# Performance work log

Hardware: AMD Instinct MI355X
Metric: run time of the kernel (lower is better)

## Reference

```python
import jax, jax.numpy as jnp
import numpy as np

H = 4  # num_heads

def setup_inputs() -> dict:
    key = jax.random.key(0)
    ks = jax.random.split(key, 9)
    B, S, D = 8, 2048, 256
    x = jax.random.normal(ks[0], (B, S, D), dtype=jnp.float32)
    scale = 1.0 / np.sqrt(D)
    Wq = jax.random.normal(ks[1], (D, D), dtype=jnp.float32) * scale
    bq = jnp.zeros((D,), dtype=jnp.float32)
    Wk = jax.random.normal(ks[2], (D, D), dtype=jnp.float32) * scale
    bk = jnp.zeros((D,), dtype=jnp.float32)
    Wv = jax.random.normal(ks[3], (D, D), dtype=jnp.float32) * scale
    bv = jnp.zeros((D,), dtype=jnp.float32)
    Wo = jax.random.normal(ks[4], (D, D), dtype=jnp.float32) * scale
    bo = jnp.zeros((D,), dtype=jnp.float32)
    return {"x": x, "Wq": Wq, "bq": bq, "Wk": Wk, "bk": bk,
            "Wv": Wv, "bv": bv, "Wo": Wo, "bo": bo}

def reference(x, Wq, bq, Wk, bk, Wv, bv, Wo, bo):
    B, S, D = x.shape
    hd = D // H
    inv_scale = 1.0 / jnp.sqrt(jnp.asarray(hd, x.dtype))
    # projections: torch Linear is x @ W.T + b; weights here stored as (D, D) used as x @ W + b
    def split_heads(t):
        return t.reshape(B, S, H, hd).transpose(0, 2, 1, 3)  # [B,H,S,hd]
    Q = split_heads(x @ Wq + bq)
    K = split_heads(x @ Wk + bk)
    V = split_heads(x @ Wv + bv)
    scores = jnp.einsum('bhqd,bhkd->bhqk', Q, K) * inv_scale  # [B,H,S,S]
    attn = jax.nn.softmax(scores, axis=-1)
    # dropout is identity in eval mode
    ctx = jnp.einsum('bhqk,bhkd->bhqd', attn, V)
    ctx = ctx.transpose(0, 2, 1, 3).reshape(B, S, D)
    return ctx @ Wo + bo
```

## Files before the change

### kernel.cpp

```cpp
#include <hip/hip_runtime.h>


typedef unsigned short u16;
typedef __bf16 bf16x8 __attribute__((ext_vector_type(8)));
typedef float  f32x4  __attribute__((ext_vector_type(4)));
typedef unsigned int u32x4 __attribute__((ext_vector_type(4)));
typedef unsigned int u32x2 __attribute__((ext_vector_type(2)));

#define LOG2E   1.4426950408889634f
#define ATTN_SC (0.125f * LOG2E)
#define PSTR    2097152
#define WPSTR   32768
#define WZSTR   65536

__device__ __forceinline__ u16 f2b(float f) {
  unsigned u = __builtin_bit_cast(unsigned, f);
  u += 0x7FFFu + ((u >> 16) & 1u);
  return (u16)(u >> 16);
}
__device__ __forceinline__ float b2f(u16 b) {
  return __builtin_bit_cast(float, (unsigned)b << 16);
}
__device__ __forceinline__ float b2f_hi(unsigned u) {
  return __builtin_bit_cast(float, u & 0xFFFF0000u);
}
__device__ __forceinline__ float b2f_lo(unsigned u) {
  return __builtin_bit_cast(float, u << 16);
}
__device__ __forceinline__ unsigned pack_trunc(float a, float b) {
  return (__builtin_bit_cast(unsigned, a) >> 16) | (__builtin_bit_cast(unsigned, b) & 0xFFFF0000u);
}
__device__ __forceinline__ unsigned pack_rne(float a, float b) {
  return (unsigned)f2b(a) | ((unsigned)f2b(b) << 16);
}
__device__ __forceinline__ f32x4 mfma16(bf16x8 a, bf16x8 b, f32x4 c) {
  return __builtin_amdgcn_mfma_f32_16x16x32_bf16(a, b, c, 0, 0, 0);
}
__device__ __forceinline__ void cp16(const u16* g, u16* l) {
  __builtin_amdgcn_global_load_lds((const __attribute__((address_space(1))) void*)g,
                                   (__attribute__((address_space(3))) void*)l, 16, 0, 0);
}

template <typename T>
__global__ __launch_bounds__(256) void prep(const T* __restrict__ x,
                                            const T* __restrict__ W0, const T* __restrict__ W1,
                                            const T* __restrict__ W2, const T* __restrict__ W3,
                                            const T* __restrict__ b0, const T* __restrict__ b1,
                                            const T* __restrict__ b2, const T* __restrict__ b3,
                                            u16* __restrict__ xp, u16* __restrict__ WTp,
                                            float* __restrict__ biasf) {
  int bid = blockIdx.x;
  if (bid < 4096) {
    int i0 = (bid * 256 + threadIdx.x) * 4;
    int row = i0 >> 8, col = i0 & 255;
    int p = col >> 7, pc = col & 127;
    u16* o = xp + (size_t)p * PSTR + (size_t)row * 128 + pc;
#pragma unroll
    for (int j = 0; j < 4; ++j) {
      if constexpr (sizeof(T) == 4) o[j] = f2b((float)x[i0 + j]);
      else                          o[j] = (u16)x[i0 + j];
    }
  } else {
    bid -= 4096;
    const int z = bid >> 8;
    const T* W = z == 0 ? W0 : z == 1 ? W1 : z == 2 ? W2 : W3;
    const T* b = z == 0 ? b0 : z == 1 ? b1 : z == 2 ? b2 : b3;
    int idx = (bid & 255) * 256 + threadIdx.x;
    int k = idx >> 8, n = idx & 255;
    u16 wb;
    if constexpr (sizeof(T) == 4) wb = f2b((float)W[k * 256 + n]);
    else                          wb = (u16)W[k * 256 + n];
    WTp[z * WZSTR + (k >> 7) * WPSTR + n * 128 + (k & 127)] = wb;
    if (idx < 256) {
      float bv;
      if constexpr (sizeof(T) == 4) bv = (float)b[idx];
      else                          bv = b2f((u16)b[idx]);
      biasf[z * 256 + idx] = bv;
    }
  }
}

__global__ __launch_bounds__(256, 2) void qkv_gemm(const u16* __restrict__ xp, const u16* __restrict__ WTp,
                                                   const float* __restrict__ biasf,
                                                   u16* __restrict__ Qw, u16* __restrict__ Kw,
                                                   u16* __restrict__ VTg) {
  __shared__ __align__(16) u16 Al[256 * 128];
  __shared__ __align__(16) u16 Bl[64 * 128];
  const int tid = threadIdx.x, w = tid >> 6, lane = tid & 63;
  const int l16 = lane & 15, quad = lane >> 4;
  const int z = blockIdx.z, n0 = blockIdx.y * 64, m0 = blockIdx.x * 256;
  const u16* Ab = xp + (size_t)m0 * 128;
  const u16* Bb = WTp + z * WZSTR + (size_t)n0 * 128;
  f32x4 acc[4][4];
#pragma unroll
  for (int mm = 0; mm < 4; ++mm)
#pragma unroll
    for (int nb = 0; nb < 4; ++nb) acc[mm][nb] = (f32x4){0.f, 0.f, 0.f, 0.f};

#pragma unroll
  for (int p = 0; p < 2; ++p) {
    __syncthreads();
    const u16* Ap = Ab + (size_t)p * PSTR;
    const u16* Bp = Bb + p * WPSTR;
#pragma unroll
    for (int i = 0; i < 16; ++i) {
      int slot = i * 256 + w * 64 + lane;
      int row = slot >> 4, pc = slot & 15, c = pc ^ (row & 15);
      cp16(Ap + (size_t)row * 128 + c * 8, Al + (i * 256 + w * 64) * 8);
    }
#pragma unroll
    for (int i = 0; i < 4; ++i) {
      int slot = i * 256 + w * 64 + lane;
      int row = slot >> 4, pc = slot & 15, c = pc ^ (row & 15);
      cp16(Bp + (size_t)row * 128 + c * 8, Bl + (i * 256 + w * 64) * 8);
    }
    __syncthreads();
#pragma unroll
    for (int kc = 0; kc < 4; ++kc) {
      int ch = ((kc * 4 + quad) ^ l16) * 8;
      bf16x8 a[4], b[4];
#pragma unroll
      for (int mm = 0; mm < 4; ++mm)
        a[mm] = *(const bf16x8*)&Al[(w * 64 + mm * 16 + l16) * 128 + ch];
#pragma unroll
      for (int nb = 0; nb < 4; ++nb)
        b[nb] = *(const bf16x8*)&Bl[(nb * 16 + l16) * 128 + ch];
#pragma unroll
      for (int mm = 0; mm < 4; ++mm)
#pragma unroll
        for (int nb = 0; nb < 4; ++nb)
          acc[mm][nb] = mfma16(a[mm], b[nb], acc[mm][nb]);
    }
  }

  const float* bp = biasf + z * 256;
  const int bb = m0 >> 11, s0 = m0 & 2047, h = blockIdx.y;
  if (z < 2) {
    u16* dst = (z == 0) ? Qw : Kw;
    const float sc = (z == 0) ? ATTN_SC : 1.0f;
#pragma unroll
    for (int mm = 0; mm < 4; ++mm)
#pragma unroll
      for (int nb = 0; nb < 4; ++nb) {
        int d = nb * 16 + l16;
        float bv = bp[n0 + d];
#pragma unroll
        for (int r = 0; r < 4; ++r) {
          int s = s0 + w * 64 + mm * 16 + quad * 4 + r;
          dst[(((size_t)(bb * 4 + h) * 2048) + s) * 64 + d] = f2b((acc[mm][nb][r] + bv) * sc);
        }
      }
  } else {
    __syncthreads();
#pragma unroll
    for (int mm = 0; mm < 4; ++mm)
#pragma unroll
      for (int nb = 0; nb < 4; ++nb) {
        int d = nb * 16 + l16;
        float bv = bp[n0 + d];
        f32x4 v = acc[mm][nb];
        u32x2 dd = { pack_rne(v[0] + bv, v[1] + bv), pack_rne(v[2] + bv, v[3] + bv) };
        int cch = w * 8 + mm * 2 + (quad >> 1);
        *(u32x2*)&Al[d * 256 + ((cch ^ (d & 31))) * 8 + (quad & 1) * 4] = dd;
      }
    __syncthreads();
#pragma unroll
    for (int i = 0; i < 8; ++i) {
      int slot = i * 256 + tid;
      int d = slot >> 5, pc = slot & 31;
      u32x4 vv = *(const u32x4*)&Al[d * 256 + ((pc ^ (d & 31))) * 8];
      *(u32x4*)(VTg + (((size_t)(bb * 4 + h) * 64) + d) * 2048 + s0 + pc * 8) = vv;
    }
  }
}

template <bool OUT_BF16>
__global__ __launch_bounds__(256) void out_gemm(const u16* __restrict__ ctxp, const u16* __restrict__ WTp,
                                                const float* __restrict__ bo, void* __restrict__ outv) {
  __shared__ __align__(16) u16 Al[128 * 128];
  __shared__ __align__(16) u16 Bl[64 * 128];
  const int tid = threadIdx.x, w = tid >> 6, lane = tid & 63;
  const int l16 = lane & 15, quad = lane >> 4;
  const int n0 = blockIdx.y * 64, m0 = blockIdx.x * 128;
  const u16* Ab = ctxp + (size_t)m0 * 128;
  const u16* Bb = WTp + 3 * WZSTR + (size_t)n0 * 128;
  f32x4 acc[2][4];
#pragma unroll
  for (int mm = 0; mm < 2; ++mm)
#pragma unroll
    for (int nb = 0; nb < 4; ++nb) acc[mm][nb] = (f32x4){0.f, 0.f, 0.f, 0.f};

#pragma unroll
  for (int p = 0; p < 2; ++p) {
    __syncthreads();
    const u16* Ap = Ab + (size_t)p * PSTR;
    const u16* Bp = Bb + p * WPSTR;
#pragma unroll
    for (int i = 0; i < 8; ++i) {
      int slot = i * 256 + w * 64 + lane;
      int row = slot >> 4, pc = slot & 15, c = pc ^ (row & 15);
      cp16(Ap + (size_t)row * 128 + c * 8, Al + (i * 256 + w * 64) * 8);
    }
#pragma unroll
    for (int i = 0; i < 4; ++i) {
      int slot = i * 256 + w * 64 + lane;
      int row = slot >> 4, pc = slot & 15, c = pc ^ (row & 15);
      cp16(Bp + (size_t)row * 128 + c * 8, Bl + (i * 256 + w * 64) * 8);
    }
    __syncthreads();
#pragma unroll
    for (int kc = 0; kc < 4; ++kc) {
      int ch = ((kc * 4 + quad) ^ l16) * 8;
      bf16x8 a0 = *(const bf16x8*)&Al[(w * 32 + l16) * 128 + ch];
      bf16x8 a1 = *(const bf16x8*)&Al[(w * 32 + 16 + l16) * 128 + ch];
#pragma unroll
      for (int nb = 0; nb < 4; ++nb) {
        bf16x8 b = *(const bf16x8*)&Bl[(nb * 16 + l16) * 128 + ch];
        acc[0][nb] = mfma16(a0, b, acc[0][nb]);
        acc[1][nb] = mfma16(a1, b, acc[1][nb]);
      }
    }
  }
#pragma unroll
  for (int mm = 0; mm < 2; ++mm)
#pragma unroll
    for (int nb = 0; nb < 4; ++nb) {
      int n = n0 + nb * 16 + l16;
      float bv = bo[n];
#pragma unroll
      for (int r = 0; r < 4; ++r) {
        size_t m = m0 + w * 32 + mm * 16 + quad * 4 + r;
        float v = acc[mm][nb][r] + bv;
        if constexpr (OUT_BF16) ((u16*)outv)[m * 256 + n] = f2b(v);
        else                    ((float*)outv)[m * 256 + n] = v;
      }
    }
}

__global__ __launch_bounds__(256, 3) void attn(const u16* __restrict__ Q, const u16* __restrict__ K,
                                               const u16* __restrict__ VT,
                                               u16* __restrict__ P0, u16* __restrict__ P1,
                                               float* __restrict__ dnb) {
  __shared__ __align__(16) u16 Kt[2][64 * 64];
  __shared__ __align__(16) u16 VTt[2][64 * 64];
  __shared__ __align__(16) u16 Pt[4][2][16 * 64];
  const int tid = threadIdx.x;
  const int w = tid >> 6, lane = tid & 63;
  const int l16 = lane & 15, quad = lane >> 4;
  const int bh = blockIdx.y, q0 = blockIdx.x * 128, z = blockIdx.z;
  const u16* Qp = Q + (size_t)bh * 2048 * 64;
  const u16* Kp = K + (size_t)bh * 2048 * 64 + (size_t)z * 1024 * 64;
  const u16* Vp = VT + (size_t)bh * 64 * 2048 + z * 1024;

  bf16x8 qf[2][2];
#pragma unroll
  for (int g = 0; g < 2; ++g) {
    int qrow = q0 + w * 32 + g * 16 + l16;
    qf[g][0] = *(const bf16x8*)(Qp + (size_t)qrow * 64 + quad * 8);
    qf[g][1] = *(const bf16x8*)(Qp + (size_t)qrow * 64 + 32 + quad * 8);
  }

  f32x4 acc[2][4];
#pragma unroll
  for (int g = 0; g < 2; ++g)
#pragma unroll
    for (int nb = 0; nb < 4; ++nb) acc[g][nb] = (f32x4){0.f, 0.f, 0.f, 0.f};
  float dn[2] = {0.f, 0.f};

  const int sl0 = tid, sl1 = 256 + tid;
  const int r0 = sl0 >> 3, c0 = (sl0 & 7) ^ (r0 & 7);
  const int r1 = sl1 >> 3, c1 = (sl1 & 7) ^ (r1 & 7);

#define STAGE(kt_, buf_)                                                                   \
  do {                                                                                     \
    cp16(Kp + (size_t)((kt_) * 64 + r0) * 64 + c0 * 8, &Kt[buf_][(w * 64) * 8]);           \
    cp16(Kp + (size_t)((kt_) * 64 + r1) * 64 + c1 * 8, &Kt[buf_][(256 + w * 64) * 8]);     \
    cp16(Vp + (size_t)r0 * 2048 + (kt_) * 64 + c0 * 8, &VTt[buf_][(w * 64) * 8]);          \
    cp16(Vp + (size_t)r1 * 2048 + (kt_) * 64 + c1 * 8, &VTt[buf_][(256 + w * 64) * 8]);    \
  } while (0)

  STAGE(0, 0);

  for (int kt = 0; kt < 16; ++kt) {
    const int buf = kt & 1;
    __builtin_amdgcn_s_waitcnt(0x0F70 );
    __asm__ __volatile__("" ::: "memory");
    __builtin_amdgcn_s_barrier();
    __asm__ __volatile__("" ::: "memory");
    if (kt < 15) STAGE(kt + 1, buf ^ 1);

    const u16* KtB = Kt[buf];
    const u16* VtB = VTt[buf];

    bf16x8 vbr[2][4];
#pragma unroll
    for (int m = 0; m < 2; ++m)
#pragma unroll
      for (int nbD = 0; nbD < 4; ++nbD)
        vbr[m][nbD] = *(const bf16x8*)&VtB[(nbD * 16 + l16) * 64 + (((m * 4 + quad) ^ (l16 & 7))) * 8];

    f32x4 st[2][4];
#pragma unroll
    for (int g = 0; g < 2; ++g)
#pragma unroll
      for (int nb = 0; nb < 4; ++nb) st[g][nb] = (f32x4){0.f, 0.f, 0.f, 0.f};
#pragma unroll
    for (int kc = 0; kc < 2; ++kc) {
#pragma unroll
      for (int nbK = 0; nbK < 4; ++nbK) {
        bf16x8 a = *(const bf16x8*)&KtB[(nbK * 16 + l16) * 64 + (((kc * 4 + quad) ^ (l16 & 7))) * 8];
        st[0][nbK] = mfma16(a, qf[0][kc], st[0][nbK]);
        st[1][nbK] = mfma16(a, qf[1][kc], st[1][nbK]);
      }
    }

#pragma unroll
    for (int g = 0; g < 2; ++g) {
      u16* Ptg = Pt[w][g];
#pragma unroll
      for (int nbK = 0; nbK < 4; ++nbK) {
        float p0 = exp2f(st[g][nbK][0]), p1 = exp2f(st[g][nbK][1]);
        float p2 = exp2f(st[g][nbK][2]), p3 = exp2f(st[g][nbK][3]);
        dn[g] += (p0 + p1) + (p2 + p3);
        u32x2 dd = { pack_trunc(p0, p1), pack_trunc(p2, p3) };
        int cch = nbK * 2 + (quad >> 1);
        *(u32x2*)&Ptg[l16 * 64 + ((cch ^ (l16 & 7))) * 8 + (quad & 1) * 4] = dd;
      }
    }

#pragma unroll
    for (int m = 0; m < 2; ++m) {
#pragma unroll
      for (int g = 0; g < 2; ++g) {
        bf16x8 pb = *(const bf16x8*)&Pt[w][g][l16 * 64 + (((m * 4 + quad) ^ (l16 & 7))) * 8];
#pragma unroll
        for (int nbD = 0; nbD < 4; ++nbD)
          acc[g][nbD] = mfma16(vbr[m][nbD], pb, acc[g][nbD]);
      }
    }
  }
#undef STAGE

  u16* pdst = z ? P1 : P0;
#pragma unroll
  for (int g = 0; g < 2; ++g) {
    float d = dn[g];
    d += __shfl_xor(d, 16);
    d += __shfl_xor(d, 32);
    dn[g] = d;
    if (quad == 0)
      dnb[z * 65536 + bh * 2048 + q0 + w * 32 + g * 16 + l16] = d;
  }

#pragma unroll
  for (int g = 0; g < 2; ++g) {
    u16* Ptg = Pt[w][g];
#pragma unroll
    for (int nbD = 0; nbD < 4; ++nbD) {
      f32x4 v = acc[g][nbD];
      u32x2 dd = { pack_rne(v[0], v[1]), pack_rne(v[2], v[3]) };
      int cch = nbD * 2 + (quad >> 1);
      *(u32x2*)&Ptg[l16 * 64 + ((cch ^ (l16 & 7))) * 8 + (quad & 1) * 4] = dd;
    }
  }
#pragma unroll
  for (int cc = 0; cc < 4; ++cc) {
    int slot = cc * 64 + lane;
    int row = slot >> 3, pc = slot & 7;
    u32x4 vv = *(const u32x4*)&Pt[w][0][row * 64 + ((pc ^ (row & 7))) * 8];
    size_t qg = q0 + w * 32 + row;
    *(u32x4*)(pdst + (((size_t)bh * 2048) + qg) * 64 + pc * 8) = vv;
  }
}

__global__ __launch_bounds__(256) void combine(const u16* __restrict__ p0, const u16* __restrict__ p1,
                                               const float* __restrict__ dnb, u16* __restrict__ ctxp) {
  int t = blockIdx.x * 256 + threadIdx.x;
  int chunk = t & 7, q = (t >> 3) & 2047, bh = t >> 14;
  size_t idx = ((((size_t)bh * 2048) + q) * 64) + chunk * 8;
  u32x4 a = *(const u32x4*)(p0 + idx);
  u32x4 b = *(const u32x4*)(p1 + idx);
  float l = 1.0f / (dnb[bh * 2048 + q] + dnb[65536 + bh * 2048 + q]);
  u32x4 o;
#pragma unroll
  for (int i = 0; i < 4; ++i) {
    float lo = (b2f_lo(a[i]) + b2f_lo(b[i])) * l;
    float hi = (b2f_hi(a[i]) + b2f_hi(b[i])) * l;
    o[i] = pack_rne(lo, hi);
  }
  int bb = bh >> 2, h = bh & 3, p = h >> 1, pcol = (h & 1) * 64;
  size_t m = (size_t)bb * 2048 + q;
  *(u32x4*)(ctxp + (size_t)p * PSTR + m * 128 + pcol + chunk * 8) = o;
}

extern "C" void kernel_launch(void* const* d_in, const int* in_sizes, int n_in,
                              void* d_out, int out_size, void* d_ws, size_t ws_size,
                              hipStream_t stream) {
  bool f32in = true;
  {
    void* basep = nullptr; size_t sz = 0;
    hipError_t e = hipMemGetAddressRange((hipDeviceptr_t*)&basep, &sz, (hipDeviceptr_t)d_in[0]);
    if (e == hipSuccess && sz > 0) f32in = sz >= (size_t)in_sizes[0] * 4;
    else f32in = false;
  }

  char* ws = (char*)d_ws;
  u16*   xp    = (u16*)(ws + 0);
  u16*   WTp   = (u16*)(ws + 8388608);
  float* biasf = (float*)(ws + 8912896);
  u16*   Qw    = (u16*)(ws + 8916992);
  u16*   Kw    = (u16*)(ws + 17305600);
  u16*   VTg   = (u16*)(ws + 25694208);
  float* dnb   = (float*)(ws + 34082816);
  u16*   part0 = xp;
  u16*   part1 = (u16*)d_out;
  u16*   ctxp  = Qw;

  if (f32in) {
    prep<float><<<5120, 256, 0, stream>>>(
        (const float*)d_in[0],
        (const float*)d_in[1], (const float*)d_in[3], (const float*)d_in[5], (const float*)d_in[7],
        (const float*)d_in[2], (const float*)d_in[4], (const float*)d_in[6], (const float*)d_in[8],
        xp, WTp, biasf);
  } else {
    prep<u16><<<5120, 256, 0, stream>>>(
        (const u16*)d_in[0],
        (const u16*)d_in[1], (const u16*)d_in[3], (const u16*)d_in[5], (const u16*)d_in[7],
        (const u16*)d_in[2], (const u16*)d_in[4], (const u16*)d_in[6], (const u16*)d_in[8],
        xp, WTp, biasf);
  }
  qkv_gemm<<<dim3(64, 4, 3), 256, 0, stream>>>(xp, WTp, biasf, Qw, Kw, VTg);
  attn<<<dim3(16, 32, 2), 256, 0, stream>>>(Qw, Kw, VTg, part0, part1, dnb);
  combine<<<2048, 256, 0, stream>>>(part0, part1, dnb, ctxp);
  if (f32in) out_gemm<false><<<dim3(128, 4), 256, 0, stream>>>(ctxp, WTp, biasf + 3 * 256, d_out);
  else       out_gemm<true ><<<dim3(128, 4), 256, 0, stream>>>(ctxp, WTp, biasf + 3 * 256, d_out);
}
```

Measured before the change: 173.6 us.

## Fuse x conversion into QKV GEMM and split-combine into output GEMM

```diff
diff --git a/kernel.cpp b/kernel.cpp
--- a/kernel.cpp
+++ b/kernel.cpp
@@ -9,7 +9,6 @@
 
 #define LOG2E   1.4426950408889634f
 #define ATTN_SC (0.125f * LOG2E)
-#define PSTR    2097152
 #define WPSTR   32768
 #define WZSTR   65536
 
@@ -42,45 +41,30 @@
 }
 
 template <typename T>
-__global__ __launch_bounds__(256) void prep(const T* __restrict__ x,
-                                            const T* __restrict__ W0, const T* __restrict__ W1,
+__global__ __launch_bounds__(256) void prep(const T* __restrict__ W0, const T* __restrict__ W1,
                                             const T* __restrict__ W2, const T* __restrict__ W3,
                                             const T* __restrict__ b0, const T* __restrict__ b1,
                                             const T* __restrict__ b2, const T* __restrict__ b3,
-                                            u16* __restrict__ xp, u16* __restrict__ WTp,
-                                            float* __restrict__ biasf) {
-  int bid = blockIdx.x;
-  if (bid < 4096) {
-    int i0 = (bid * 256 + threadIdx.x) * 4;
-    int row = i0 >> 8, col = i0 & 255;
-    int p = col >> 7, pc = col & 127;
-    u16* o = xp + (size_t)p * PSTR + (size_t)row * 128 + pc;
-#pragma unroll
-    for (int j = 0; j < 4; ++j) {
-      if constexpr (sizeof(T) == 4) o[j] = f2b((float)x[i0 + j]);
-      else                          o[j] = (u16)x[i0 + j];
-    }
-  } else {
-    bid -= 4096;
-    const int z = bid >> 8;
-    const T* W = z == 0 ? W0 : z == 1 ? W1 : z == 2 ? W2 : W3;
-    const T* b = z == 0 ? b0 : z == 1 ? b1 : z == 2 ? b2 : b3;
-    int idx = (bid & 255) * 256 + threadIdx.x;
-    int k = idx >> 8, n = idx & 255;
-    u16 wb;
-    if constexpr (sizeof(T) == 4) wb = f2b((float)W[k * 256 + n]);
-    else                          wb = (u16)W[k * 256 + n];
-    WTp[z * WZSTR + (k >> 7) * WPSTR + n * 128 + (k & 127)] = wb;
-    if (idx < 256) {
-      float bv;
-      if constexpr (sizeof(T) == 4) bv = (float)b[idx];
-      else                          bv = b2f((u16)b[idx]);
-      biasf[z * 256 + idx] = bv;
-    }
-  }
-}
-
-__global__ __launch_bounds__(256, 2) void qkv_gemm(const u16* __restrict__ xp, const u16* __restrict__ WTp,
+                                            u16* __restrict__ WTp, float* __restrict__ biasf) {
+  const int z = blockIdx.x >> 8;
+  const T* W = z == 0 ? W0 : z == 1 ? W1 : z == 2 ? W2 : W3;
+  const T* b = z == 0 ? b0 : z == 1 ? b1 : z == 2 ? b2 : b3;
+  int idx = (blockIdx.x & 255) * 256 + threadIdx.x;
+  int k = idx >> 8, n = idx & 255;
+  u16 wb;
+  if constexpr (sizeof(T) == 4) wb = f2b((float)W[k * 256 + n]);
+  else                          wb = (u16)W[k * 256 + n];
+  WTp[z * WZSTR + (k >> 7) * WPSTR + n * 128 + (k & 127)] = wb;
+  if (idx < 256) {
+    float bv;
+    if constexpr (sizeof(T) == 4) bv = (float)b[idx];
+    else                          bv = b2f((u16)b[idx]);
+    biasf[z * 256 + idx] = bv;
+  }
+}
+
+template <typename T>
+__global__ __launch_bounds__(256, 2) void qkv_gemm(const T* __restrict__ x, const u16* __restrict__ WTp,
                                                    const float* __restrict__ biasf,
                                                    u16* __restrict__ Qw, u16* __restrict__ Kw,
                                                    u16* __restrict__ VTg) {
@@ -89,7 +73,6 @@
   const int tid = threadIdx.x, w = tid >> 6, lane = tid & 63;
   const int l16 = lane & 15, quad = lane >> 4;
   const int z = blockIdx.z, n0 = blockIdx.y * 64, m0 = blockIdx.x * 256;
-  const u16* Ab = xp + (size_t)m0 * 128;
   const u16* Bb = WTp + z * WZSTR + (size_t)n0 * 128;
   f32x4 acc[4][4];
 #pragma unroll
@@ -100,19 +83,28 @@
 #pragma unroll
   for (int p = 0; p < 2; ++p) {
     __syncthreads();
-    const u16* Ap = Ab + (size_t)p * PSTR;
     const u16* Bp = Bb + p * WPSTR;
 #pragma unroll
     for (int i = 0; i < 16; ++i) {
-      int slot = i * 256 + w * 64 + lane;
+      int slot = i * 256 + tid;
       int row = slot >> 4, pc = slot & 15, c = pc ^ (row & 15);
-      cp16(Ap + (size_t)row * 128 + c * 8, Al + (i * 256 + w * 64) * 8);
+      const T* src = x + (size_t)(m0 + row) * 256 + p * 128 + c * 8;
+      u32x4 dd;
+      if constexpr (sizeof(T) == 4) {
+        f32x4 v0 = *(const f32x4*)src;
+        f32x4 v1 = *(const f32x4*)(src + 4);
+        dd = (u32x4){ pack_rne(v0[0], v0[1]), pack_rne(v0[2], v0[3]),
+                      pack_rne(v1[0], v1[1]), pack_rne(v1[2], v1[3]) };
+      } else {
+        dd = *(const u32x4*)src;
+      }
+      *(u32x4*)&Al[slot * 8] = dd;
     }
 #pragma unroll
     for (int i = 0; i < 4; ++i) {
-      int slot = i * 256 + w * 64 + lane;
+      int slot = i * 256 + tid;
       int row = slot >> 4, pc = slot & 15, c = pc ^ (row & 15);
-      cp16(Bp + (size_t)row * 128 + c * 8, Bl + (i * 256 + w * 64) * 8);
+      cp16(Bp + (size_t)row * 128 + c * 8, Bl + slot * 8);
     }
     __syncthreads();
 #pragma unroll
@@ -174,76 +166,13 @@
   }
 }
 
-template <bool OUT_BF16>
-__global__ __launch_bounds__(256) void out_gemm(const u16* __restrict__ ctxp, const u16* __restrict__ WTp,
-                                                const float* __restrict__ bo, void* __restrict__ outv) {
-  __shared__ __align__(16) u16 Al[128 * 128];
-  __shared__ __align__(16) u16 Bl[64 * 128];
-  const int tid = threadIdx.x, w = tid >> 6, lane = tid & 63;
-  const int l16 = lane & 15, quad = lane >> 4;
-  const int n0 = blockIdx.y * 64, m0 = blockIdx.x * 128;
-  const u16* Ab = ctxp + (size_t)m0 * 128;
-  const u16* Bb = WTp + 3 * WZSTR + (size_t)n0 * 128;
-  f32x4 acc[2][4];
-#pragma unroll
-  for (int mm = 0; mm < 2; ++mm)
-#pragma unroll
-    for (int nb = 0; nb < 4; ++nb) acc[mm][nb] = (f32x4){0.f, 0.f, 0.f, 0.f};
-
-#pragma unroll
-  for (int p = 0; p < 2; ++p) {
-    __syncthreads();
-    const u16* Ap = Ab + (size_t)p * PSTR;
-    const u16* Bp = Bb + p * WPSTR;
-#pragma unroll
-    for (int i = 0; i < 8; ++i) {
-      int slot = i * 256 + w * 64 + lane;
-      int row = slot >> 4, pc = slot & 15, c = pc ^ (row & 15);
-      cp16(Ap + (size_t)row * 128 + c * 8, Al + (i * 256 + w * 64) * 8);
-    }
-#pragma unroll
-    for (int i = 0; i < 4; ++i) {
-      int slot = i * 256 + w * 64 + lane;
-      int row = slot >> 4, pc = slot & 15, c = pc ^ (row & 15);
-      cp16(Bp + (size_t)row * 128 + c * 8, Bl + (i * 256 + w * 64) * 8);
-    }
-    __syncthreads();
-#pragma unroll
-    for (int kc = 0; kc < 4; ++kc) {
-      int ch = ((kc * 4 + quad) ^ l16) * 8;
-      bf16x8 a0 = *(const bf16x8*)&Al[(w * 32 + l16) * 128 + ch];
-      bf16x8 a1 = *(const bf16x8*)&Al[(w * 32 + 16 + l16) * 128 + ch];
-#pragma unroll
-      for (int nb = 0; nb < 4; ++nb) {
-        bf16x8 b = *(const bf16x8*)&Bl[(nb * 16 + l16) * 128 + ch];
-        acc[0][nb] = mfma16(a0, b, acc[0][nb]);
-        acc[1][nb] = mfma16(a1, b, acc[1][nb]);
-      }
-    }
-  }
-#pragma unroll
-  for (int mm = 0; mm < 2; ++mm)
-#pragma unroll
-    for (int nb = 0; nb < 4; ++nb) {
-      int n = n0 + nb * 16 + l16;
-      float bv = bo[n];
-#pragma unroll
-      for (int r = 0; r < 4; ++r) {
-        size_t m = m0 + w * 32 + mm * 16 + quad * 4 + r;
-        float v = acc[mm][nb][r] + bv;
-        if constexpr (OUT_BF16) ((u16*)outv)[m * 256 + n] = f2b(v);
-        else                    ((float*)outv)[m * 256 + n] = v;
-      }
-    }
-}
-
-__global__ __launch_bounds__(256, 3) void attn(const u16* __restrict__ Q, const u16* __restrict__ K,
+__global__ __launch_bounds__(256, 4) void attn(const u16* __restrict__ Q, const u16* __restrict__ K,
                                                const u16* __restrict__ VT,
                                                u16* __restrict__ P0, u16* __restrict__ P1,
                                                float* __restrict__ dnb) {
   __shared__ __align__(16) u16 Kt[2][64 * 64];
   __shared__ __align__(16) u16 VTt[2][64 * 64];
-  __shared__ __align__(16) u16 Pt[4][2][16 * 64];
+  __shared__ __align__(16) u16 Pt[4][16 * 64];
   const int tid = threadIdx.x;
   const int w = tid >> 6, lane = tid & 63;
   const int l16 = lane & 15, quad = lane >> 4;
@@ -251,6 +180,7 @@
   const u16* Qp = Q + (size_t)bh * 2048 * 64;
   const u16* Kp = K + (size_t)bh * 2048 * 64 + (size_t)z * 1024 * 64;
   const u16* Vp = VT + (size_t)bh * 64 * 2048 + z * 1024;
+  u16* Ptw = Pt[w];
 
   bf16x8 qf[2][2];
 #pragma unroll
@@ -292,13 +222,6 @@
     const u16* KtB = Kt[buf];
     const u16* VtB = VTt[buf];
 
-    bf16x8 vbr[2][4];
-#pragma unroll
-    for (int m = 0; m < 2; ++m)
-#pragma unroll
-      for (int nbD = 0; nbD < 4; ++nbD)
-        vbr[m][nbD] = *(const bf16x8*)&VtB[(nbD * 16 + l16) * 64 + (((m * 4 + quad) ^ (l16 & 7))) * 8];
-
     f32x4 st[2][4];
 #pragma unroll
     for (int g = 0; g < 2; ++g)
@@ -314,9 +237,15 @@
       }
     }
 
+    bf16x8 vbr[2][4];
+#pragma unroll
+    for (int m = 0; m < 2; ++m)
+#pragma unroll
+      for (int nbD = 0; nbD < 4; ++nbD)
+        vbr[m][nbD] = *(const bf16x8*)&VtB[(nbD * 16 + l16) * 64 + (((m * 4 + quad) ^ (l16 & 7))) * 8];
+
 #pragma unroll
     for (int g = 0; g < 2; ++g) {
-      u16* Ptg = Pt[w][g];
 #pragma unroll
       for (int nbK = 0; nbK < 4; ++nbK) {
         float p0 = exp2f(st[g][nbK][0]), p1 = exp2f(st[g][nbK][1]);
@@ -324,15 +253,11 @@
         dn[g] += (p0 + p1) + (p2 + p3);
         u32x2 dd = { pack_trunc(p0, p1), pack_trunc(p2, p3) };
         int cch = nbK * 2 + (quad >> 1);
-        *(u32x2*)&Ptg[l16 * 64 + ((cch ^ (l16 & 7))) * 8 + (quad & 1) * 4] = dd;
-      }
-    }
-
-#pragma unroll
-    for (int m = 0; m < 2; ++m) {
-#pragma unroll
-      for (int g = 0; g < 2; ++g) {
-        bf16x8 pb = *(const bf16x8*)&Pt[w][g][l16 * 64 + (((m * 4 + quad) ^ (l16 & 7))) * 8];
+        *(u32x2*)&Ptw[l16 * 64 + ((cch ^ (l16 & 7))) * 8 + (quad & 1) * 4] = dd;
+      }
+#pragma unroll
+      for (int m = 0; m < 2; ++m) {
+        bf16x8 pb = *(const bf16x8*)&Ptw[l16 * 64 + (((m * 4 + quad) ^ (l16 & 7))) * 8];
 #pragma unroll
         for (int nbD = 0; nbD < 4; ++nbD)
           acc[g][nbD] = mfma16(vbr[m][nbD], pb, acc[g][nbD]);
@@ -347,34 +272,32 @@
     float d = dn[g];
     d += __shfl_xor(d, 16);
     d += __shfl_xor(d, 32);
-    dn[g] = d;
     if (quad == 0)
       dnb[z * 65536 + bh * 2048 + q0 + w * 32 + g * 16 + l16] = d;
   }
 
 #pragma unroll
   for (int g = 0; g < 2; ++g) {
-    u16* Ptg = Pt[w][g];
 #pragma unroll
     for (int nbD = 0; nbD < 4; ++nbD) {
       f32x4 v = acc[g][nbD];
       u32x2 dd = { pack_rne(v[0], v[1]), pack_rne(v[2], v[3]) };
       int cch = nbD * 2 + (quad >> 1);
-      *(u32x2*)&Ptg[l16 * 64 + ((cch ^ (l16 & 7))) * 8 + (quad & 1) * 4] = dd;
-    }
-  }
-#pragma unroll
-  for (int cc = 0; cc < 4; ++cc) {
-    int slot = cc * 64 + lane;
-    int row = slot >> 3, pc = slot & 7;
-    u32x4 vv = *(const u32x4*)&Pt[w][0][row * 64 + ((pc ^ (row & 7))) * 8];
-    size_t qg = q0 + w * 32 + row;
-    *(u32x4*)(pdst + (((size_t)bh * 2048) + qg) * 64 + pc * 8) = vv;
+      *(u32x2*)&Ptw[l16 * 64 + ((cch ^ (l16 & 7))) * 8 + (quad & 1) * 4] = dd;
+    }
+#pragma unroll
+    for (int cc = 0; cc < 2; ++cc) {
+      int slot = cc * 64 + lane;
+      int row = slot >> 3, pc = slot & 7;
+      u32x4 vv = *(const u32x4*)&Ptw[row * 64 + ((pc ^ (row & 7))) * 8];
+      size_t qg = q0 + w * 32 + g * 16 + row;
+      *(u32x4*)(pdst + (((size_t)bh * 2048) + qg) * 64 + pc * 8) = vv;
+    }
   }
 }
 
 __global__ __launch_bounds__(256) void combine(const u16* __restrict__ p0, const u16* __restrict__ p1,
-                                               const float* __restrict__ dnb, u16* __restrict__ ctxp) {
+                                               const float* __restrict__ dnb, u16* __restrict__ ctxc) {
   int t = blockIdx.x * 256 + threadIdx.x;
   int chunk = t & 7, q = (t >> 3) & 2047, bh = t >> 14;
   size_t idx = ((((size_t)bh * 2048) + q) * 64) + chunk * 8;
@@ -388,9 +311,85 @@
     float hi = (b2f_hi(a[i]) + b2f_hi(b[i])) * l;
     o[i] = pack_rne(lo, hi);
   }
-  int bb = bh >> 2, h = bh & 3, p = h >> 1, pcol = (h & 1) * 64;
-  size_t m = (size_t)bb * 2048 + q;
-  *(u32x4*)(ctxp + (size_t)p * PSTR + m * 128 + pcol + chunk * 8) = o;
+  *(u32x4*)(ctxc + idx) = o;
+}
+
+template <bool OUT_BF16, bool MERGED>
+__global__ __launch_bounds__(256) void out_gemm(const u16* __restrict__ p0, const u16* __restrict__ p1,
+                                                const float* __restrict__ dnb,
+                                                const u16* __restrict__ WTp,
+                                                const float* __restrict__ bo, void* __restrict__ outv) {
+  __shared__ __align__(16) u16 Al[128 * 128];
+  __shared__ __align__(16) u16 Bl[64 * 128];
+  const int tid = threadIdx.x, w = tid >> 6, lane = tid & 63;
+  const int l16 = lane & 15, quad = lane >> 4;
+  const int n0 = blockIdx.y * 64, m0 = blockIdx.x * 128;
+  const u16* Bb = WTp + 3 * WZSTR + (size_t)n0 * 128;
+  f32x4 acc[2][4];
+#pragma unroll
+  for (int mm = 0; mm < 2; ++mm)
+#pragma unroll
+    for (int nb = 0; nb < 4; ++nb) acc[mm][nb] = (f32x4){0.f, 0.f, 0.f, 0.f};
+
+#pragma unroll
+  for (int p = 0; p < 2; ++p) {
+    __syncthreads();
+    const u16* Bp = Bb + p * WPSTR;
+#pragma unroll
+    for (int i = 0; i < 8; ++i) {
+      int slot = i * 256 + tid;
+      int row = slot >> 4, pc = slot & 15, c = pc ^ (row & 15);
+      int m = m0 + row, bb = m >> 11, q = m & 2047;
+      int col0 = p * 128 + c * 8, h = col0 >> 6, d0 = col0 & 63;
+      size_t idx = (((size_t)(bb * 4 + h) * 2048) + q) * 64 + d0;
+      u32x4 dd;
+      if constexpr (MERGED) {
+        u32x4 a = *(const u32x4*)(p0 + idx);
+        u32x4 b = *(const u32x4*)(p1 + idx);
+        float l = 1.0f / (dnb[(bb * 4 + h) * 2048 + q] + dnb[65536 + (bb * 4 + h) * 2048 + q]);
+#pragma unroll
+        for (int j = 0; j < 4; ++j)
+          dd[j] = pack_rne((b2f_lo(a[j]) + b2f_lo(b[j])) * l,
+                           (b2f_hi(a[j]) + b2f_hi(b[j])) * l);
+      } else {
+        dd = *(const u32x4*)(p0 + idx);
+      }
+      *(u32x4*)&Al[slot * 8] = dd;
+    }
+#pragma unroll
+    for (int i = 0; i < 4; ++i) {
+      int slot = i * 256 + tid;
+      int row = slot >> 4, pc = slot & 15, c = pc ^ (row & 15);
+      cp16(Bp + (size_t)row * 128 + c * 8, Bl + slot * 8);
+    }
+    __syncthreads();
+#pragma unroll
+    for (int kc = 0; kc < 4; ++kc) {
+      int ch = ((kc * 4 + quad) ^ l16) * 8;
+      bf16x8 a0 = *(const bf16x8*)&Al[(w * 32 + l16) * 128 + ch];
+      bf16x8 a1 = *(const bf16x8*)&Al[(w * 32 + 16 + l16) * 128 + ch];
+#pragma unroll
+      for (int nb = 0; nb < 4; ++nb) {
+        bf16x8 b = *(const bf16x8*)&Bl[(nb * 16 + l16) * 128 + ch];
+        acc[0][nb] = mfma16(a0, b, acc[0][nb]);
+        acc[1][nb] = mfma16(a1, b, acc[1][nb]);
+      }
+    }
+  }
+#pragma unroll
+  for (int mm = 0; mm < 2; ++mm)
+#pragma unroll
+    for (int nb = 0; nb < 4; ++nb) {
+      int n = n0 + nb * 16 + l16;
+      float bv = bo[n];
+#pragma unroll
+      for (int r = 0; r < 4; ++r) {
+        size_t m = m0 + w * 32 + mm * 16 + quad * 4 + r;
+        float v = acc[mm][nb][r] + bv;
+        if constexpr (OUT_BF16) ((u16*)outv)[m * 256 + n] = f2b(v);
+        else                    ((float*)outv)[m * 256 + n] = v;
+      }
+    }
 }
 
 extern "C" void kernel_launch(void* const* d_in, const int* in_sizes, int n_in,
@@ -405,33 +404,38 @@
   }
 
   char* ws = (char*)d_ws;
-  u16*   xp    = (u16*)(ws + 0);
+  u16*   p0    = (u16*)(ws + 0);
   u16*   WTp   = (u16*)(ws + 8388608);
   float* biasf = (float*)(ws + 8912896);
   u16*   Qw    = (u16*)(ws + 8916992);
   u16*   Kw    = (u16*)(ws + 17305600);
   u16*   VTg   = (u16*)(ws + 25694208);
   float* dnb   = (float*)(ws + 34082816);
-  u16*   part0 = xp;
-  u16*   part1 = (u16*)d_out;
-  u16*   ctxp  = Qw;
+  const size_t P1_OFF = 34607104;
+  bool fused = ws_size >= P1_OFF + 8388608;
+  u16* p1 = fused ? (u16*)(ws + P1_OFF) : (u16*)d_out;
+  u16* ctxc = Qw;
 
   if (f32in) {
-    prep<float><<<5120, 256, 0, stream>>>(
-        (const float*)d_in[0],
+    prep<float><<<1024, 256, 0, stream>>>(
         (const float*)d_in[1], (const float*)d_in[3], (const float*)d_in[5], (const float*)d_in[7],
         (const float*)d_in[2], (const float*)d_in[4], (const float*)d_in[6], (const float*)d_in[8],
-        xp, WTp, biasf);
+        WTp, biasf);
+    qkv_gemm<float><<<dim3(64, 4, 3), 256, 0, stream>>>((const float*)d_in[0], WTp, biasf, Qw, Kw, VTg);
   } else {
-    prep<u16><<<5120, 256, 0, stream>>>(
-        (const u16*)d_in[0],
+    prep<u16><<<1024, 256, 0, stream>>>(
         (const u16*)d_in[1], (const u16*)d_in[3], (const u16*)d_in[5], (const u16*)d_in[7],
         (const u16*)d_in[2], (const u16*)d_in[4], (const u16*)d_in[6], (const u16*)d_in[8],
-        xp, WTp, biasf);
-  }
-  qkv_gemm<<<dim3(64, 4, 3), 256, 0, stream>>>(xp, WTp, biasf, Qw, Kw, VTg);
-  attn<<<dim3(16, 32, 2), 256, 0, stream>>>(Qw, Kw, VTg, part0, part1, dnb);
-  combine<<<2048, 256, 0, stream>>>(part0, part1, dnb, ctxp);
-  if (f32in) out_gemm<false><<<dim3(128, 4), 256, 0, stream>>>(ctxp, WTp, biasf + 3 * 256, d_out);
-  else       out_gemm<true ><<<dim3(128, 4), 256, 0, stream>>>(ctxp, WTp, biasf + 3 * 256, d_out);
-}
+        WTp, biasf);
+    qkv_gemm<u16><<<dim3(64, 4, 3), 256, 0, stream>>>((const u16*)d_in[0], WTp, biasf, Qw, Kw, VTg);
+  }
+  attn<<<dim3(16, 32, 2), 256, 0, stream>>>(Qw, Kw, VTg, p0, p1, dnb);
+  if (fused) {
+    if (f32in) out_gemm<false, true><<<dim3(128, 4), 256, 0, stream>>>(p0, p1, dnb, WTp, biasf + 3 * 256, d_out);
+    else       out_gemm<true,  true><<<dim3(128, 4), 256, 0, stream>>>(p0, p1, dnb, WTp, biasf + 3 * 256, d_out);
+  } else {
+    combine<<<2048, 256, 0, stream>>>(p0, p1, dnb, ctxc);
+    if (f32in) out_gemm<false, false><<<dim3(128, 4), 256, 0, stream>>>(ctxc, nullptr, dnb, WTp, biasf + 3 * 256, d_out);
+    else       out_gemm<true,  false><<<dim3(128, 4), 256, 0, stream>>>(ctxc, nullptr, dnb, WTp, biasf + 3 * 256, d_out);
+  }
+}
```

Result: faster. 169.1 us (-2.6%).
